# Kernel tuning notes

Measured on AMD Instinct MI355X. Metric: run time of the kernel, lower is better.

Reference implementation:

```python
import jax, jax.numpy as jnp
import numpy as np

MEMDIM, MEMSIZE, NHEADS = 1024, 32768, 8
B, S = 2, 512

def setup_inputs() -> dict:
    key = jax.random.key(0)
    k1, k2, k3 = jax.random.split(key, 3)
    h = jax.random.normal(k1, (B, S, MEMDIM), dtype=jnp.float32)
    # mimic nn.Linear default init scale (~U(-1/sqrt(fan_in),1/sqrt(fan_in))) via small normals
    keys_w = jax.random.normal(k2, (MEMSIZE, MEMDIM), dtype=jnp.float32) * (1.0 / np.sqrt(MEMDIM))
    values_w = jax.random.normal(k3, (MEMDIM, MEMSIZE), dtype=jnp.float32) * (1.0 / np.sqrt(MEMSIZE))
    return {"h": h, "keys_w": keys_w, "values_w": values_w}

def reference(h, keys_w, values_w):
    hd = MEMDIM // NHEADS  # per-head dim
    # queries: [b, s, h, d]
    q = h.reshape(*h.shape[:-1], NHEADS, hd)
    # keys.weight [memsize, memdim] -> [z, h, d]
    k = keys_w.reshape(MEMSIZE, NHEADS, hd)
    # scores [b, s, h, z]; note: original has NO 1/sqrt(d) scaling
    w = jnp.einsum('bshd,zhd->bshz', q, k)
    w = jax.nn.softmax(w, axis=-1)
    # values.weight [memdim, memsize] -> [h, d, z]
    v = values_w.reshape(NHEADS, hd, MEMSIZE)
    ret = jnp.einsum('bshz,hdz->bshd', w, v)
    return ret.reshape(*ret.shape[:-2], MEMDIM)
```

## Files before the change

kernel.cpp:

```cpp
#include <hip/hip_runtime.h>
#include <hip/hip_bf16.h>


#define NH 8
#define HD 128
#define LQ 1024
#define ZTOT 32768
#define ZSPLIT 4
#define ZCHUNK (ZTOT / ZSPLIT)
#define ZSTEP 64
#define MQ 128
#define QT (LQ / MQ)
#define LOG2E 1.44269504088896f

typedef __bf16 bf16x8 __attribute__((ext_vector_type(8)));
typedef float f32x4 __attribute__((ext_vector_type(4)));

#define K_BASE 0
#define V_BASE 16384
#define P_BASE 32768

__device__ __forceinline__ bf16x8 to_bf8(float4 a, float4 b) {
    bf16x8 r;
    r[0] = (__bf16)a.x; r[1] = (__bf16)a.y; r[2] = (__bf16)a.z; r[3] = (__bf16)a.w;
    r[4] = (__bf16)b.x; r[5] = (__bf16)b.y; r[6] = (__bf16)b.z; r[7] = (__bf16)b.w;
    return r;
}

__global__ __launch_bounds__(512) void kvmem_flash(
    const float* __restrict__ hin, const float* __restrict__ kw,
    const float* __restrict__ vw, float* __restrict__ Opart,
    float* __restrict__ Mpart, float* __restrict__ Lpart)
{
    __shared__ __align__(16) unsigned char smem[49152];

    const int bid  = blockIdx.x;
    const int head = bid >> 5;
    const int zs   = (bid >> 3) & 3;
    const int qt   = bid & 7;
    const int tid  = threadIdx.x;
    const int wv   = tid >> 6;
    const int ln   = tid & 63;
    const int l15  = ln & 15;
    const int lg   = ln >> 4;

    const int zbase0 = zs * ZCHUNK;
    const int qrow0  = qt * MQ;

    bf16x8 qf[4];
    {
        const float* qsrc = hin + (size_t)(qrow0 + wv * 16 + l15) * 1024 + head * HD;
        #pragma unroll
        for (int kf = 0; kf < 4; ++kf) {
            const float4* p4 = reinterpret_cast<const float4*>(qsrc + kf * 32 + lg * 8);
            qf[kf] = to_bf8(p4[0], p4[1]);
        }
    }

    f32x4 oacc[8];
    #pragma unroll
    for (int i = 0; i < 8; ++i) oacc[i] = f32x4{0.f, 0.f, 0.f, 0.f};
    float mrow[4], lrow[4];
    #pragma unroll
    for (int r = 0; r < 4; ++r) { mrow[r] = -1e30f; lrow[r] = 0.f; }

    const unsigned pbase = P_BASE + wv * 2048;

    for (int zb = 0; zb < ZCHUNK; zb += ZSTEP) {
        __syncthreads();

        #pragma unroll
        for (int pp = 0; pp < 2; ++pp) {
            int c = tid + pp * 512;
            int z = c >> 4, dc = c & 15;
            const float4* src = reinterpret_cast<const float4*>(
                kw + (size_t)(zbase0 + zb + z) * 1024 + head * HD + dc * 8);
            unsigned byte = (unsigned)(z * 256 + dc * 16) ^ ((unsigned)(z & 7) << 4);
            *(bf16x8*)(smem + K_BASE + byte) = to_bf8(src[0], src[1]);
        }
        #pragma unroll
        for (int pp = 0; pp < 2; ++pp) {
            int c = tid + pp * 512;
            int d = c >> 3, zc = c & 7;
            const float4* src = reinterpret_cast<const float4*>(
                vw + (size_t)(head * HD + d) * 32768 + zbase0 + zb + zc * 8);
            unsigned byte = (unsigned)(d * 128 + zc * 16) ^ ((unsigned)(d & 7) << 4);
            *(bf16x8*)(smem + V_BASE + byte) = to_bf8(src[0], src[1]);
        }
        __syncthreads();

        f32x4 sf[4];
        #pragma unroll
        for (int cf = 0; cf < 4; ++cf) sf[cf] = f32x4{0.f, 0.f, 0.f, 0.f};
        #pragma unroll
        for (int kf = 0; kf < 4; ++kf) {
            #pragma unroll
            for (int cf = 0; cf < 4; ++cf) {
                int z = cf * 16 + l15;
                unsigned byte = (unsigned)(z * 256 + (kf * 32 + lg * 8) * 2)
                                ^ ((unsigned)(z & 7) << 4);
                bf16x8 b = *(const bf16x8*)(smem + K_BASE + byte);
                sf[cf] = __builtin_amdgcn_mfma_f32_16x16x32_bf16(qf[kf], b, sf[cf], 0, 0, 0);
            }
        }

        float scale[4], psum[4];
        #pragma unroll
        for (int r = 0; r < 4; ++r) {
            float mx = fmaxf(fmaxf(sf[0][r], sf[1][r]), fmaxf(sf[2][r], sf[3][r]));
            #pragma unroll
            for (int msk = 1; msk < 16; msk <<= 1) mx = fmaxf(mx, __shfl_xor(mx, msk, 16));
            float mn = fmaxf(mrow[r], mx);
            scale[r] = exp2f((mrow[r] - mn) * LOG2E);
            mrow[r] = mn;
            psum[r] = 0.f;
        }
        #pragma unroll
        for (int cf = 0; cf < 4; ++cf) {
            #pragma unroll
            for (int r = 0; r < 4; ++r) {
                float p = exp2f((sf[cf][r] - mrow[r]) * LOG2E);
                psum[r] += p;
                int row = lg * 4 + r;
                unsigned byte = (unsigned)(row * 128 + (cf * 16 + l15) * 2)
                                ^ ((unsigned)(row & 7) << 4);
                *(__bf16*)(smem + pbase + byte) = (__bf16)p;
            }
        }
        #pragma unroll
        for (int r = 0; r < 4; ++r) {
            float s = psum[r];
            #pragma unroll
            for (int msk = 1; msk < 16; msk <<= 1) s += __shfl_xor(s, msk, 16);
            lrow[r] = lrow[r] * scale[r] + s;
        }
        #pragma unroll
        for (int df = 0; df < 8; ++df) {
            #pragma unroll
            for (int r = 0; r < 4; ++r) oacc[df][r] *= scale[r];
        }

        #pragma unroll
        for (int kf2 = 0; kf2 < 2; ++kf2) {
            unsigned abyte = (unsigned)(l15 * 128 + (kf2 * 32 + lg * 8) * 2)
                             ^ ((unsigned)(l15 & 7) << 4);
            bf16x8 pa = *(const bf16x8*)(smem + pbase + abyte);
            #pragma unroll
            for (int df = 0; df < 8; ++df) {
                int d = df * 16 + l15;
                unsigned byte = (unsigned)(d * 128 + (kf2 * 32 + lg * 8) * 2)
                                ^ ((unsigned)(d & 7) << 4);
                bf16x8 vb = *(const bf16x8*)(smem + V_BASE + byte);
                oacc[df] = __builtin_amdgcn_mfma_f32_16x16x32_bf16(pa, vb, oacc[df], 0, 0, 0);
            }
        }
    }

    const int sb = (zs * NH + head) * LQ;
    #pragma unroll
    for (int df = 0; df < 8; ++df) {
        #pragma unroll
        for (int r = 0; r < 4; ++r) {
            int row = qrow0 + wv * 16 + lg * 4 + r;
            Opart[(size_t)(sb + row) * HD + df * 16 + l15] = oacc[df][r];
        }
    }
    if (l15 == 0) {
        #pragma unroll
        for (int r = 0; r < 4; ++r) {
            int row = qrow0 + wv * 16 + lg * 4 + r;
            Mpart[sb + row] = mrow[r];
            Lpart[sb + row] = lrow[r];
        }
    }
}

__global__ __launch_bounds__(128) void kvmem_combine(
    const float* __restrict__ Opart, const float* __restrict__ Mpart,
    const float* __restrict__ Lpart, float* __restrict__ out)
{
    const int bid  = blockIdx.x;
    const int head = bid >> 10;
    const int row  = bid & 1023;
    const int d    = threadIdx.x;

    float m[ZSPLIT];
    float M = -1e30f;
    #pragma unroll
    for (int z = 0; z < ZSPLIT; ++z) {
        m[z] = Mpart[(z * NH + head) * LQ + row];
        M = fmaxf(M, m[z]);
    }
    float L = 0.f, o = 0.f;
    #pragma unroll
    for (int z = 0; z < ZSPLIT; ++z) {
        float w = exp2f((m[z] - M) * LOG2E);
        L += w * Lpart[(z * NH + head) * LQ + row];
        o += w * Opart[(size_t)((z * NH + head) * LQ + row) * HD + d];
    }
    out[(size_t)row * 1024 + head * HD + d] = o / L;
}

extern "C" void kernel_launch(void* const* d_in, const int* in_sizes, int n_in,
                              void* d_out, int out_size, void* d_ws, size_t ws_size,
                              hipStream_t stream) {
    const float* hin = (const float*)d_in[0];
    const float* kw  = (const float*)d_in[1];
    const float* vw  = (const float*)d_in[2];
    float* out = (float*)d_out;

    float* Opart = (float*)d_ws;
    float* Mpart = Opart + (size_t)ZSPLIT * NH * LQ * HD;
    float* Lpart = Mpart + ZSPLIT * NH * LQ;

    kvmem_flash<<<dim3(NH * QT * ZSPLIT), dim3(512), 0, stream>>>(
        hin, kw, vw, Opart, Mpart, Lpart);
    kvmem_combine<<<dim3(NH * LQ), dim3(HD), 0, stream>>>(Opart, Mpart, Lpart, out);
}
```

Measured before the change: 855.7 us.

## Double-buffer K/V tiles with register prefetch and remap block order

Prefetches the next K/V tile from global memory into registers while the current tile's MFMAs run, then converts it and stores it into a second LDS buffer, so each iteration needs one barrier instead of two. It also remaps block indices so that blocks sharing the same head and z-chunk (and thus the same K/V data) are adjacent, and switches exp2f to the hardware exp2 builtin. Shared memory grows to 80KB and register use rises from the staging buffers, which may lower occupancy.

```diff
diff --git a/kernel.cpp b/kernel.cpp
--- a/kernel.cpp
+++ b/kernel.cpp
@@ -9,6 +9,7 @@
 #define ZSPLIT 4
 #define ZCHUNK (ZTOT / ZSPLIT)
 #define ZSTEP 64
+#define NT (ZCHUNK / ZSTEP)
 #define MQ 128
 #define QT (LQ / MQ)
 #define LOG2E 1.44269504088896f
@@ -16,9 +17,9 @@
 typedef __bf16 bf16x8 __attribute__((ext_vector_type(8)));
 typedef float f32x4 __attribute__((ext_vector_type(4)));
 
-#define K_BASE 0
-#define V_BASE 16384
-#define P_BASE 32768
+#define KB(b) ((b) * 32768)
+#define VB(b) ((b) * 32768 + 16384)
+#define P_BASE 65536
 
 __device__ __forceinline__ bf16x8 to_bf8(float4 a, float4 b) {
     bf16x8 r;
@@ -32,20 +33,38 @@
     const float* __restrict__ vw, float* __restrict__ Opart,
     float* __restrict__ Mpart, float* __restrict__ Lpart)
 {
-    __shared__ __align__(16) unsigned char smem[49152];
-
-    const int bid  = blockIdx.x;
-    const int head = bid >> 5;
-    const int zs   = (bid >> 3) & 3;
-    const int qt   = bid & 7;
-    const int tid  = threadIdx.x;
-    const int wv   = tid >> 6;
-    const int ln   = tid & 63;
-    const int l15  = ln & 15;
-    const int lg   = ln >> 4;
+    __shared__ __align__(16) unsigned char smem[81920];
+
+    const int bid = blockIdx.x;
+    const int x    = bid & 7;
+    const int qt   = (bid >> 3) & 7;
+    const int ghi  = bid >> 6;
+    const int g    = x + (ghi << 3);
+    const int head = g >> 2;
+    const int zs   = g & 3;
+
+    const int tid = threadIdx.x;
+    const int wv  = tid >> 6;
+    const int ln  = tid & 63;
+    const int l15 = ln & 15;
+    const int lg  = ln >> 4;
 
     const int zbase0 = zs * ZCHUNK;
     const int qrow0  = qt * MQ;
+
+    const int kz = tid >> 4, kd = tid & 15;
+    const int vd = tid >> 3, vz = tid & 7;
+    const float* kbase = kw + (size_t)(zbase0 + kz) * 1024 + head * HD + kd * 8;
+    const float* vbase = vw + (size_t)(head * HD + vd) * 32768 + zbase0 + vz * 8;
+
+    unsigned kwb[2], vwb[2];
+    #pragma unroll
+    for (int pp = 0; pp < 2; ++pp) {
+        int z = kz + pp * 32;
+        kwb[pp] = (unsigned)(z * 256 + kd * 16) ^ ((unsigned)(z & 7) << 4);
+        int d = vd + pp * 64;
+        vwb[pp] = (unsigned)(d * 128 + vz * 16) ^ ((unsigned)(d & 7) << 4);
+    }
 
     bf16x8 qf[4];
     {
@@ -66,28 +85,37 @@
 
     const unsigned pbase = P_BASE + wv * 2048;
 
-    for (int zb = 0; zb < ZCHUNK; zb += ZSTEP) {
-        __syncthreads();
-
-        #pragma unroll
-        for (int pp = 0; pp < 2; ++pp) {
-            int c = tid + pp * 512;
-            int z = c >> 4, dc = c & 15;
-            const float4* src = reinterpret_cast<const float4*>(
-                kw + (size_t)(zbase0 + zb + z) * 1024 + head * HD + dc * 8);
-            unsigned byte = (unsigned)(z * 256 + dc * 16) ^ ((unsigned)(z & 7) << 4);
-            *(bf16x8*)(smem + K_BASE + byte) = to_bf8(src[0], src[1]);
-        }
-        #pragma unroll
-        for (int pp = 0; pp < 2; ++pp) {
-            int c = tid + pp * 512;
-            int d = c >> 3, zc = c & 7;
-            const float4* src = reinterpret_cast<const float4*>(
-                vw + (size_t)(head * HD + d) * 32768 + zbase0 + zb + zc * 8);
-            unsigned byte = (unsigned)(d * 128 + zc * 16) ^ ((unsigned)(d & 7) << 4);
-            *(bf16x8*)(smem + V_BASE + byte) = to_bf8(src[0], src[1]);
-        }
-        __syncthreads();
+    float4 kst[4], vst[4];
+
+    #pragma unroll
+    for (int pp = 0; pp < 2; ++pp) {
+        const float4* ks = reinterpret_cast<const float4*>(kbase + (size_t)pp * 32 * 1024);
+        kst[2 * pp] = ks[0]; kst[2 * pp + 1] = ks[1];
+        const float4* vs = reinterpret_cast<const float4*>(vbase + (size_t)pp * 64 * 32768);
+        vst[2 * pp] = vs[0]; vst[2 * pp + 1] = vs[1];
+    }
+    #pragma unroll
+    for (int pp = 0; pp < 2; ++pp) {
+        *(bf16x8*)(smem + KB(0) + kwb[pp]) = to_bf8(kst[2 * pp], kst[2 * pp + 1]);
+        *(bf16x8*)(smem + VB(0) + vwb[pp]) = to_bf8(vst[2 * pp], vst[2 * pp + 1]);
+    }
+    __syncthreads();
+
+    for (int it = 0; it < NT; ++it) {
+        const int cur = it & 1;
+
+        if (it + 1 < NT) {
+            const size_t zo = (size_t)(it + 1) * ZSTEP;
+            #pragma unroll
+            for (int pp = 0; pp < 2; ++pp) {
+                const float4* ks = reinterpret_cast<const float4*>(
+                    kbase + (zo + pp * 32) * 1024);
+                kst[2 * pp] = ks[0]; kst[2 * pp + 1] = ks[1];
+                const float4* vs = reinterpret_cast<const float4*>(
+                    vbase + zo + (size_t)pp * 64 * 32768);
+                vst[2 * pp] = vs[0]; vst[2 * pp + 1] = vs[1];
+            }
+        }
 
         f32x4 sf[4];
         #pragma unroll
@@ -99,7 +127,7 @@
                 int z = cf * 16 + l15;
                 unsigned byte = (unsigned)(z * 256 + (kf * 32 + lg * 8) * 2)
                                 ^ ((unsigned)(z & 7) << 4);
-                bf16x8 b = *(const bf16x8*)(smem + K_BASE + byte);
+                bf16x8 b = *(const bf16x8*)(smem + KB(cur) + byte);
                 sf[cf] = __builtin_amdgcn_mfma_f32_16x16x32_bf16(qf[kf], b, sf[cf], 0, 0, 0);
             }
         }
@@ -111,7 +139,7 @@
             #pragma unroll
             for (int msk = 1; msk < 16; msk <<= 1) mx = fmaxf(mx, __shfl_xor(mx, msk, 16));
             float mn = fmaxf(mrow[r], mx);
-            scale[r] = exp2f((mrow[r] - mn) * LOG2E);
+            scale[r] = __builtin_amdgcn_exp2f((mrow[r] - mn) * LOG2E);
             mrow[r] = mn;
             psum[r] = 0.f;
         }
@@ -119,7 +147,7 @@
         for (int cf = 0; cf < 4; ++cf) {
             #pragma unroll
             for (int r = 0; r < 4; ++r) {
-                float p = exp2f((sf[cf][r] - mrow[r]) * LOG2E);
+                float p = __builtin_amdgcn_exp2f((sf[cf][r] - mrow[r]) * LOG2E);
                 psum[r] += p;
                 int row = lg * 4 + r;
                 unsigned byte = (unsigned)(row * 128 + (cf * 16 + l15) * 2)
@@ -150,10 +178,19 @@
                 int d = df * 16 + l15;
                 unsigned byte = (unsigned)(d * 128 + (kf2 * 32 + lg * 8) * 2)
                                 ^ ((unsigned)(d & 7) << 4);
-                bf16x8 vb = *(const bf16x8*)(smem + V_BASE + byte);
+                bf16x8 vb = *(const bf16x8*)(smem + VB(cur) + byte);
                 oacc[df] = __builtin_amdgcn_mfma_f32_16x16x32_bf16(pa, vb, oacc[df], 0, 0, 0);
             }
         }
+
+        if (it + 1 < NT) {
+            #pragma unroll
+            for (int pp = 0; pp < 2; ++pp) {
+                *(bf16x8*)(smem + KB(cur ^ 1) + kwb[pp]) = to_bf8(kst[2 * pp], kst[2 * pp + 1]);
+                *(bf16x8*)(smem + VB(cur ^ 1) + vwb[pp]) = to_bf8(vst[2 * pp], vst[2 * pp + 1]);
+            }
+        }
+        __syncthreads();
     }
 
     const int sb = (zs * NH + head) * LQ;
@@ -194,7 +231,7 @@
     float L = 0.f, o = 0.f;
     #pragma unroll
     for (int z = 0; z < ZSPLIT; ++z) {
-        float w = exp2f((m[z] - M) * LOG2E);
+        float w = __builtin_amdgcn_exp2f((m[z] - M) * LOG2E);
         L += w * Lpart[(z * NH + head) * LQ + row];
         o += w * Opart[(size_t)((z * NH + head) * LQ + row) * HD + d];
     }
```

New measurement: 782.1 us. -8.6%, faster.
